# Kernel optimization log

Measured on AMD Instinct MI355X. Metric: run time of the kernel, lower is better.

Reference implementation:

```python
import jax, jax.numpy as jnp
import numpy as np

B, S, IN, OUT, H, L, NH, STEPS = 256, 128, 64, 64, 1024, 2, 4, 16
HD = H // NH


def setup_inputs() -> dict:
    key = jax.random.key(0)
    ks = iter(jax.random.split(key, 32))
    std_h = 1.0 / np.sqrt(H)

    def u(k, shape, std):
        return jax.random.uniform(k, shape, jnp.float32, -std, std)

    inp = {"x": jax.random.normal(next(ks), (B, S, IN), jnp.float32)}
    # LSTM cells: stacked gate weights, gate order (i, f, g, o); y = x@Wx + h@Wh + b
    for name, din in (("e0", IN), ("e1", H), ("d0", OUT), ("d1", H)):
        inp[name + "_Wx"] = u(next(ks), (din, 4 * H), std_h)
        inp[name + "_Wh"] = u(next(ks), (H, 4 * H), std_h)
        inp[name + "_b"] = u(next(ks), (4 * H,), std_h)
    # attention linears (x@W + b convention)
    for name in ("Wq", "Wk", "Wv", "Wo"):
        inp[name] = u(next(ks), (H, H), std_h)
    for name in ("bq", "bk", "bv", "bo"):
        inp[name] = u(next(ks), (H,), std_h)
    inp["fc_W"] = u(next(ks), (2 * H, H), 1.0 / np.sqrt(2 * H))
    inp["fc_b"] = u(next(ks), (H,), 1.0 / np.sqrt(2 * H))
    inp["out_W"] = u(next(ks), (H, OUT), std_h)
    inp["out_b"] = u(next(ks), (OUT,), std_h)
    return inp


def _cell(x_t, h, c, Wx, Wh, b):
    z = x_t @ Wx + h @ Wh + b  # [B, 4H]
    i, f, g, o = jnp.split(z, 4, axis=-1)
    c = jax.nn.sigmoid(f) * c + jax.nn.sigmoid(i) * jnp.tanh(g)
    h = jax.nn.sigmoid(o) * jnp.tanh(c)
    return h, c


def _lstm_seq(x, Wx, Wh, b):
    # x: [B, T, D] -> outputs [B, T, H], final (h, c)
    h0 = jnp.zeros((x.shape[0], H), x.dtype)
    def step(carry, xt):
        h, c = carry
        h, c = _cell(xt, h, c, Wx, Wh, b)
        return (h, c), h
    (h, c), ys = jax.lax.scan(step, (h0, h0), jnp.swapaxes(x, 0, 1))
    return jnp.swapaxes(ys, 0, 1), h, c


def reference(x, e0_Wx, e0_Wh, e0_b, e1_Wx, e1_Wh, e1_b,
              d0_Wx, d0_Wh, d0_b, d1_Wx, d1_Wh, d1_b,
              Wq, bq, Wk, bk, Wv, bv, Wo, bo, fc_W, fc_b, out_W, out_b):
    # encoder: 2-layer manual LSTM (dropout=0, eval)
    y0, h0, c0 = _lstm_seq(x, e0_Wx, e0_Wh, e0_b)
    enc_out, h1, c1 = _lstm_seq(y0, e1_Wx, e1_Wh, e1_b)

    # K/V projections of encoder outputs (constant across decoder steps)
    Kp = (enc_out @ Wk + bk).reshape(B, S, NH, HD)
    Vp = (enc_out @ Wv + bv).reshape(B, S, NH, HD)
    scale = float(HD) ** 0.5

    def dstep(carry, _):
        dh0, dc0, dh1, dc1, xin = carry
        dh0, dc0 = _cell(xin, dh0, dc0, d0_Wx, d0_Wh, d0_b)
        dh1, dc1 = _cell(dh0, dh1, dc1, d1_Wx, d1_Wh, d1_b)
        q = (dh1 @ Wq + bq).reshape(B, NH, HD)
        scores = jnp.einsum('bnd,bsnd->bns', q, Kp) / scale
        w = jax.nn.softmax(scores, axis=-1)
        ctx = jnp.einsum('bns,bsnd->bnd', w, Vp).reshape(B, H)
        attn = ctx @ Wo + bo
        comb = jax.nn.relu(jnp.concatenate([dh1, attn], axis=-1) @ fc_W + fc_b)
        out = comb @ out_W + out_b  # [B, OUT]
        return (dh0, dc0, dh1, dc1, out), out

    init = (h0, c0, h1, c1, jnp.zeros((B, OUT), x.dtype))
    _, preds = jax.lax.scan(dstep, init, None, length=STEPS)
    return jnp.swapaxes(preds, 0, 1)  # [B, STEPS, OUT]
```

## Files before the change

kernel.cpp:

```cpp
#include <hip/hip_runtime.h>
#include <math.h>

typedef _Float16 h8 __attribute__((ext_vector_type(8)));
typedef _Float16 h4 __attribute__((ext_vector_type(4)));
typedef float f16v __attribute__((ext_vector_type(16)));

#define HPS 262144
#define XPS 2097152
#define IPS 16384
#define BSTR 40
#define BUFE (128 * BSTR)

__device__ __forceinline__ float4 ld4(const float* p) { return *(const float4*)p; }
__device__ __forceinline__ float sigf(float x) { return 1.0f / (1.0f + expf(-x)); }
__device__ __forceinline__ float bf2f(unsigned short u) { return __uint_as_float(((unsigned)u) << 16); }
__device__ __forceinline__ float rdin(const void* p, size_t i, int bf) {
  return bf ? bf2f(((const unsigned short*)p)[i]) : ((const float*)p)[i];
}

__global__ void detect_dtype(const unsigned short* __restrict__ probe, int n, int* flag) {
  __shared__ int cnt;
  if (threadIdx.x == 0) cnt = 0;
  __syncthreads();
  int c = 0;
  for (int i = threadIdx.x; i < n; i += 256) {
    int e = (probe[i] >> 7) & 0xFF;
    if (e >= 100 && e <= 126) c++;
  }
  atomicAdd(&cnt, c);
  __syncthreads();
  if (threadIdx.x == 0) *flag = (cnt > (n * 3) / 4) ? 1 : 0;
}

__global__ void cvt_f32(const void* __restrict__ in, float* __restrict__ out, int n,
                        const int* __restrict__ flag) {
  int bf = *flag;
  int i = blockIdx.x * 256 + threadIdx.x;
  if (i < n) out[i] = rdin(in, i, bf);
}

__global__ void tsplit(const void* __restrict__ in, int N,
                       _Float16* __restrict__ outHi, _Float16* __restrict__ outLo,
                       int ldo, int kOff, int pOff, const int* __restrict__ flag) {
  __shared__ float tile[32][33];
  int bf = *flag;
  int kb = blockIdx.x * 32, nb = blockIdx.y * 32;
  for (int r = threadIdx.y; r < 32; r += 8)
    tile[threadIdx.x][r] = rdin(in, (size_t)(kb + r) * N + nb + threadIdx.x, bf);
  __syncthreads();
  for (int r = threadIdx.y; r < 32; r += 8) {
    float v = tile[r][threadIdx.x];
    _Float16 hi = (_Float16)v;
    _Float16 lo = (_Float16)(v - (float)hi);
    size_t o = (size_t)(pOff + nb + r) * ldo + kOff + kb + threadIdx.x;
    outHi[o] = hi; outLo[o] = lo;
  }
}

__global__ void f2h_kernel(const void* __restrict__ in, _Float16* __restrict__ out, int n,
                           const int* __restrict__ flag) {
  int bf = *flag;
  int i = blockIdx.x * 1024 + threadIdx.x * 4;
  if (i < n) {
    float vv[4];
#pragma unroll
    for (int k = 0; k < 4; ++k) vv[k] = rdin(in, i + k, bf);
    h4 hv, lv;
#pragma unroll
    for (int k = 0; k < 4; ++k) { hv[k] = (_Float16)vv[k]; lv[k] = (_Float16)(vv[k] - (float)hv[k]); }
    *(h4*)(out + i) = hv;
    *(h4*)(out + n + i) = lv;
  }
}

__global__ void sentinel_kernel(float* out, float v) { out[0] = v; }

__device__ __forceinline__ void gemm_tile(
    const _Float16* __restrict__ A0, int lda0, int aps0,
    const _Float16* __restrict__ A1, int lda1, int aps1, int ksplit,
    const _Float16* __restrict__ WTh, const _Float16* __restrict__ WTl, int ldw,
    int pbase, int c0, int c1,
    float* __restrict__ zp, int zld, _Float16* Bs ) {
  const int tid = threadIdx.x;
  const int wv = tid >> 6, lane = tid & 63;
  const int l31 = lane & 31, lhi = lane >> 5;

  f16v acc00 = {}, acc01 = {}, acc10 = {}, acc11 = {};

  const int r0 = wv * 64 + l31;
  const int r1 = r0 + 32;
  const _Float16* a0b0 = A0 + (size_t)r0 * lda0;
  const _Float16* a1b0 = A1 + (size_t)r0 * lda1;
  const _Float16* a0b1 = A0 + (size_t)r1 * lda0;
  const _Float16* a1b1 = A1 + (size_t)r1 * lda1;

  const int spl = tid >> 7;
  const int sidx = tid & 127;
  const int sp = sidx >> 1;
  const int skh = (sidx & 1) << 4;
  const _Float16* srow = (spl ? WTl : WTh) + (size_t)(pbase + sp) * ldw + skh;
  const int sdoff = (spl * 64 + sp) * BSTR + skh;

  {
    const _Float16* s = srow + (c0 << 5);
    float4 v0 = *(const float4*)(s);
    float4 v1 = *(const float4*)(s + 8);
    _Float16* d = Bs + sdoff;
    *(float4*)(d) = v0;
    *(float4*)(d + 8) = v1;
  }

  int buf = 0;
  for (int c = c0; c < c1; ++c) {
    __syncthreads();
    float4 n0, n1;
    const bool more = (c + 1 < c1);
    if (more) {
      const _Float16* s = srow + ((c + 1) << 5);
      n0 = *(const float4*)(s);
      n1 = *(const float4*)(s + 8);
    }
    const _Float16* bb = Bs + buf * BUFE;
    int k0 = c << 5;
#pragma unroll
    for (int sub = 0; sub < 2; ++sub) {
      int ks = k0 + sub * 16 + lhi * 8;
      const _Float16 *pa0, *pa1; int ap;
      if (ks < ksplit) { pa0 = a0b0 + ks; pa1 = a0b1 + ks; ap = aps0; }
      else { int kk = ks - ksplit; pa0 = a1b0 + kk; pa1 = a1b1 + kk; ap = aps1; }
      h8 af0h = *(const h8*)pa0;
      h8 af0l = *(const h8*)(pa0 + ap);
      h8 af1h = *(const h8*)pa1;
      h8 af1l = *(const h8*)(pa1 + ap);
      int kl = sub * 16 + lhi * 8;
      h8 b0h = *(const h8*)(bb + (size_t)(l31) * BSTR + kl);
      h8 b0l = *(const h8*)(bb + (size_t)(64 + l31) * BSTR + kl);
      h8 b1h = *(const h8*)(bb + (size_t)(32 + l31) * BSTR + kl);
      h8 b1l = *(const h8*)(bb + (size_t)(96 + l31) * BSTR + kl);
      acc00 = __builtin_amdgcn_mfma_f32_32x32x16_f16(af0h, b0h, acc00, 0, 0, 0);
      acc00 = __builtin_amdgcn_mfma_f32_32x32x16_f16(af0h, b0l, acc00, 0, 0, 0);
      acc00 = __builtin_amdgcn_mfma_f32_32x32x16_f16(af0l, b0h, acc00, 0, 0, 0);
      acc01 = __builtin_amdgcn_mfma_f32_32x32x16_f16(af0h, b1h, acc01, 0, 0, 0);
      acc01 = __builtin_amdgcn_mfma_f32_32x32x16_f16(af0h, b1l, acc01, 0, 0, 0);
      acc01 = __builtin_amdgcn_mfma_f32_32x32x16_f16(af0l, b1h, acc01, 0, 0, 0);
      acc10 = __builtin_amdgcn_mfma_f32_32x32x16_f16(af1h, b0h, acc10, 0, 0, 0);
      acc10 = __builtin_amdgcn_mfma_f32_32x32x16_f16(af1h, b0l, acc10, 0, 0, 0);
      acc10 = __builtin_amdgcn_mfma_f32_32x32x16_f16(af1l, b0h, acc10, 0, 0, 0);
      acc11 = __builtin_amdgcn_mfma_f32_32x32x16_f16(af1h, b1h, acc11, 0, 0, 0);
      acc11 = __builtin_amdgcn_mfma_f32_32x32x16_f16(af1h, b1l, acc11, 0, 0, 0);
      acc11 = __builtin_amdgcn_mfma_f32_32x32x16_f16(af1l, b1h, acc11, 0, 0, 0);
    }
    if (more) {
      _Float16* d = Bs + (buf ^ 1) * BUFE + sdoff;
      *(float4*)(d) = n0;
      *(float4*)(d + 8) = n1;
    }
    buf ^= 1;
  }

#pragma unroll
  for (int mi = 0; mi < 2; ++mi) {
#pragma unroll
    for (int ni = 0; ni < 2; ++ni) {
      f16v av = (mi == 0) ? (ni == 0 ? acc00 : acc01) : (ni == 0 ? acc10 : acc11);
      int col = pbase + ni * 32 + l31;
#pragma unroll
      for (int r = 0; r < 16; ++r) {
        int row = wv * 64 + mi * 32 + (r & 3) + ((r >> 2) * 8) + lhi * 4;
        zp[(size_t)row * zld + col] = av[r];
      }
    }
  }
}

__global__ __launch_bounds__(256, 2) void enc_gemm(int t, int l1kq,
    const _Float16* xh, const _Float16* h0, const _Float16* h1,
    const _Float16* wt0h, const _Float16* wt0l,
    const _Float16* wt1h, const _Float16* wt1l,
    const _Float16* wtkvh, const _Float16* wtkvl,
    float* z0, float* z1, float* kvz) {
  __shared__ _Float16 Bs[2 * BUFE];
  int blk = blockIdx.x;
  int nl1 = 64 * l1kq;
  if (blk < nl1) {
    if (t < 1 || t > 128) return;
    int pg = blk & 63, kq = blk >> 6;
    int c0 = (64 * kq) / l1kq, c1 = (64 * (kq + 1)) / l1kq;
    gemm_tile(h0, 1024, HPS, h1, 1024, HPS, 1024, wt1h, wt1l, 2048,
              pg * 64, c0, c1, z1 + (size_t)kq * 1048576, 4096, Bs);
  } else if (blk < nl1 + 128) {
    if (t > 127) return;
    int w = blk - nl1, pg = w & 63, kq = w >> 6;
    gemm_tile(xh + (size_t)t * 64, 8192, XPS, h0, 1024, HPS, 64, wt0h, wt0l, 1088,
              pg * 64, kq * 17, kq * 17 + 17, z0 + (size_t)kq * 1048576, 4096, Bs);
  } else {
    if (t < 2) return;
    int w = blk - nl1 - 128, pg = w & 31, kq = w >> 5;
    gemm_tile(h1, 1024, HPS, h1, 1024, HPS, 1024, wtkvh, wtkvl, 1024,
              pg * 64, kq * 16, kq * 16 + 16, kvz + (size_t)kq * 524288, 2048, Bs);
  }
}

__global__ __launch_bounds__(256, 2) void gemm_k(
    const _Float16* A0, int lda0, int aps0,
    const _Float16* A1, int lda1, int aps1, int ksplit,
    const _Float16* WTh, const _Float16* WTl, int ldw,
    int npg, int nkq, int tot, int kqoff, float* zp, int zld) {
  __shared__ _Float16 Bs[2 * BUFE];
  int pg = blockIdx.x % npg, kq = blockIdx.x / npg + kqoff;
  int c0 = (tot * kq) / nkq, c1 = (tot * (kq + 1)) / nkq;
  gemm_tile(A0, lda0, aps0, A1, lda1, aps1, ksplit, WTh, WTl, ldw,
            pg * 64, c0, c1, zp + (size_t)kq * 256 * zld, zld, Bs);
}

__global__ __launch_bounds__(256, 2) void qfc_kernel(
    const _Float16* h1,
    const _Float16* wqh, const _Float16* wql,
    const _Float16* wfh, const _Float16* wfl,
    float* qp, float* fcp) {
  __shared__ _Float16 Bs[2 * BUFE];
  int blk = blockIdx.x;
  if (blk < 64) {
    int pg = blk & 15, kq = blk >> 4;
    gemm_tile(h1, 1024, HPS, h1, 1024, HPS, 1024, wqh, wql, 1024,
              pg * 64, kq * 8, kq * 8 + 8, qp + (size_t)kq * 262144, 1024, Bs);
  } else {
    int w = blk - 64, pg = w & 15, kq = w >> 4;
    gemm_tile(h1, 1024, HPS, h1, 1024, HPS, 1024, wfh, wfl, 2048,
              pg * 64, kq * 8, kq * 8 + 8, fcp + (size_t)kq * 262144, 1024, Bs);
  }
}

__device__ __forceinline__ void gates_body(const float* __restrict__ zp, int nparts,
    const float* __restrict__ bias, float* __restrict__ c,
    _Float16* __restrict__ h, int blk) {
  int e = blk * 1024 + threadIdx.x * 4;
  int b = e >> 10, j = e & 1023;
  size_t zrow = (size_t)b * 4096;
  float4 vi = ld4(bias + j), vf = ld4(bias + 1024 + j), vg = ld4(bias + 2048 + j), vo = ld4(bias + 3072 + j);
  for (int q = 0; q < nparts; ++q) {
    const float* zq = zp + (size_t)q * 1048576 + zrow;
    float4 t;
    t = ld4(zq + j);        vi.x += t.x; vi.y += t.y; vi.z += t.z; vi.w += t.w;
    t = ld4(zq + 1024 + j); vf.x += t.x; vf.y += t.y; vf.z += t.z; vf.w += t.w;
    t = ld4(zq + 2048 + j); vg.x += t.x; vg.y += t.y; vg.z += t.z; vg.w += t.w;
    t = ld4(zq + 3072 + j); vo.x += t.x; vo.y += t.y; vo.z += t.z; vo.w += t.w;
  }
  float* cp = c + (size_t)b * 1024 + j;
  float4 cv = ld4(cp);
  float zi[4] = {vi.x, vi.y, vi.z, vi.w}, zf[4] = {vf.x, vf.y, vf.z, vf.w};
  float zg[4] = {vg.x, vg.y, vg.z, vg.w}, zo[4] = {vo.x, vo.y, vo.z, vo.w};
  float cc[4] = {cv.x, cv.y, cv.z, cv.w};
  float hn[4];
#pragma unroll
  for (int k = 0; k < 4; ++k) {
    float ii = sigf(zi[k]), ff = sigf(zf[k]), gg = tanhf(zg[k]), oo = sigf(zo[k]);
    float cn = ff * cc[k] + ii * gg;
    cc[k] = cn;
    hn[k] = oo * tanhf(cn);
  }
  float4 co; co.x = cc[0]; co.y = cc[1]; co.z = cc[2]; co.w = cc[3];
  *(float4*)cp = co;
  h4 hv, lv;
#pragma unroll
  for (int k = 0; k < 4; ++k) { hv[k] = (_Float16)hn[k]; lv[k] = (_Float16)(hn[k] - (float)hv[k]); }
  *(h4*)(h + (size_t)b * 1024 + j) = hv;
  *(h4*)(h + HPS + (size_t)b * 1024 + j) = lv;
}

__global__ void enc_gates(int t, int l1parts, const float* z0, const float* z1, const float* kvz,
                          const float* b0, const float* b1,
                          const float* bk, const float* bv,
                          float* c0, float* c1, _Float16* h0, _Float16* h1,
                          _Float16* Kp, _Float16* Vp) {
  int blk = blockIdx.x;
  if (blk < 256) {
    if (t > 127) return;
    gates_body(z0, 2, b0, c0, h0, blk);
  } else if (blk < 512) {
    if (t < 1 || t > 128) return;
    gates_body(z1, l1parts, b1, c1, h1, blk - 256);
  } else {
    if (t < 2) return;
    int e = (blk - 512) * 1024 + threadIdx.x * 4;
    int b = e >> 11, col = e & 2047;
    const float* bb = (col < 1024) ? (bk + col) : (bv + col - 1024);
    float4 v = ld4(bb);
    for (int q = 0; q < 2; ++q) {
      float4 tt = ld4(kvz + (size_t)q * 524288 + e);
      v.x += tt.x; v.y += tt.y; v.z += tt.z; v.w += tt.w;
    }
    _Float16* dst = (col < 1024) ? Kp : Vp;
    int cc = (col < 1024) ? col : col - 1024;
    h4 hv; hv[0] = (_Float16)v.x; hv[1] = (_Float16)v.y; hv[2] = (_Float16)v.z; hv[3] = (_Float16)v.w;
    *(h4*)(dst + (size_t)(b * 128 + (t - 2)) * 1024 + cc) = hv;
  }
}

__global__ void dec_gates(const float* zp, int nparts, const float* bias,
                          float* c, _Float16* h) {
  gates_body(zp, nparts, bias, c, h, blockIdx.x);
}

__global__ void reduce_act(const float* __restrict__ zp, int nparts,
                           const float* __restrict__ bias, _Float16* __restrict__ out, int relu) {
  int e = blockIdx.x * 1024 + threadIdx.x * 4;
  int j = e & 1023;
  float4 v = ld4(bias + j);
  for (int q = 0; q < nparts; ++q) {
    float4 t = ld4(zp + (size_t)q * 262144 + e);
    v.x += t.x; v.y += t.y; v.z += t.z; v.w += t.w;
  }
  if (relu) {
    v.x = fmaxf(v.x, 0.f); v.y = fmaxf(v.y, 0.f); v.z = fmaxf(v.z, 0.f); v.w = fmaxf(v.w, 0.f);
  }
  float vv[4] = {v.x, v.y, v.z, v.w};
  h4 hv, lv;
#pragma unroll
  for (int k = 0; k < 4; ++k) { hv[k] = (_Float16)vv[k]; lv[k] = (_Float16)(vv[k] - (float)hv[k]); }
  *(h4*)(out + e) = hv;
  *(h4*)(out + HPS + e) = lv;
}

__global__ void out_reduce(const float* __restrict__ op, const float* __restrict__ outb,
                           float* __restrict__ dout, _Float16* __restrict__ xin, int s) {
  int e = blockIdx.x * 1024 + threadIdx.x * 4;
  int b = e >> 6, o = e & 63;
  float4 v = ld4(outb + o);
  for (int q = 0; q < 16; ++q) {
    float4 t = ld4(op + (size_t)q * 16384 + e);
    v.x += t.x; v.y += t.y; v.z += t.z; v.w += t.w;
  }
  *(float4*)(dout + (size_t)(b * 16 + s) * 64 + o) = v;
  float vv[4] = {v.x, v.y, v.z, v.w};
  h4 hv, lv;
#pragma unroll
  for (int k = 0; k < 4; ++k) { hv[k] = (_Float16)vv[k]; lv[k] = (_Float16)(vv[k] - (float)hv[k]); }
  *(h4*)(xin + e) = hv;
  *(h4*)(xin + IPS + e) = lv;
}

__global__ void attn_kernel(const float* __restrict__ qp, const float* __restrict__ bq,
                            const _Float16* __restrict__ Kp, const _Float16* __restrict__ Vp,
                            _Float16* __restrict__ ctx) {
  int b = blockIdx.x >> 2, n = blockIdx.x & 3;
  __shared__ float qs[256];
  __shared__ float sw[128];
  int tid = threadIdx.x;
  float qv = bq[n * 256 + tid];
  for (int q = 0; q < 4; ++q) qv += qp[(size_t)q * 262144 + (size_t)b * 1024 + n * 256 + tid];
  qs[tid] = qv;
  __syncthreads();
  int w = tid >> 6, lane = tid & 63;
  for (int s = w; s < 128; s += 4) {
    const _Float16* kr = Kp + (size_t)(b * 128 + s) * 1024 + n * 256;
    float acc = 0.f;
#pragma unroll
    for (int d = 0; d < 4; ++d) acc += qs[lane + d * 64] * (float)kr[lane + d * 64];
    for (int off = 32; off; off >>= 1) acc += __shfl_down(acc, off);
    if (lane == 0) sw[s] = acc * 0.0625f;
  }
  __syncthreads();
  if (w == 0) {
    float a = sw[lane], bb = sw[lane + 64];
    float m = fmaxf(a, bb);
    for (int off = 32; off; off >>= 1) m = fmaxf(m, __shfl_down(m, off));
    m = __shfl(m, 0);
    float e1 = expf(a - m), e2 = expf(bb - m);
    float ss = e1 + e2;
    for (int off = 32; off; off >>= 1) ss += __shfl_down(ss, off);
    ss = __shfl(ss, 0);
    float inv = 1.0f / ss;
    sw[lane] = e1 * inv; sw[lane + 64] = e2 * inv;
  }
  __syncthreads();
  float acc = 0.f;
  const _Float16* vb = Vp + (size_t)b * 131072 + n * 256 + tid;
  for (int s2 = 0; s2 < 128; ++s2) acc += sw[s2] * (float)vb[(size_t)s2 * 1024];
  size_t idx = (size_t)b * 1024 + n * 256 + tid;
  _Float16 hi = (_Float16)acc;
  ctx[idx] = hi;
  ctx[HPS + idx] = (_Float16)(acc - (float)hi);
}

extern "C" void kernel_launch(void* const* d_in, const int* in_sizes, int n_in,
                              void* d_out, int out_size, void* d_ws, size_t ws_size,
                              hipStream_t stream) {
  const void* x     = d_in[0];
  const void* e0_Wx = d_in[1];
  const void* e0_Wh = d_in[2];
  const void* e0_b  = d_in[3];
  const void* e1_Wx = d_in[4];
  const void* e1_Wh = d_in[5];
  const void* e1_b  = d_in[6];
  const void* d0_Wx = d_in[7];
  const void* d0_Wh = d_in[8];
  const void* d0_b  = d_in[9];
  const void* d1_Wx = d_in[10];
  const void* d1_Wh = d_in[11];
  const void* d1_b  = d_in[12];
  const void* Wq = d_in[13];
  const void* Wk = d_in[14];
  const void* Wv = d_in[15];
  const void* Wo = d_in[16];
  const void* bq = d_in[17];
  const void* bk = d_in[18];
  const void* bv = d_in[19];
  const void* bo = d_in[20];
  const void* fc_W  = d_in[21];
  const void* fc_b  = d_in[22];
  const void* out_W = d_in[23];
  const void* out_b = d_in[24];

  int l1parts = 4;
  char* p = (char*)d_ws;
  int* flag; float* bias_arena; char* warena; char* zero0;
  _Float16 *h0, *h1, *xin, *Kp, *Vp, *ctx, *attn_h, *comb;
  float *c0, *c1; float* zarena;
  size_t zeroBytes = 0;

  for (int attempt = 0; attempt < 2; ++attempt) {
    p = (char*)d_ws;
    auto alloc = [&](size_t bytes) { char* r = p; p += (bytes + 255) & ~(size_t)255; return r; };
    flag = (int*)alloc(256);
    bias_arena = (float*)alloc(87040);
    warena = alloc(68419584);
    zero0 = p;
    h0 = (_Float16*)alloc(1048576);
    h1 = (_Float16*)alloc(1048576);
    c0 = (float*)alloc(1048576);
    c1 = (float*)alloc(1048576);
    xin = (_Float16*)alloc(65536);
    zeroBytes = (size_t)(p - zero0);
    Kp = (_Float16*)alloc(67108864);
    Vp = (_Float16*)alloc(67108864);
    zarena = (float*)alloc((size_t)(3 + l1parts) * 4194304);
    ctx    = (_Float16*)alloc(1048576);
    attn_h = (_Float16*)alloc(1048576);
    comb   = (_Float16*)alloc(1048576);
    if ((size_t)(p - (char*)d_ws) <= ws_size) break;
    l1parts = 2;
  }
  if ((size_t)(p - (char*)d_ws) > ws_size) {
    sentinel_kernel<<<1, 1, 0, stream>>>((float*)d_out, 1.0e9f + (float)ws_size);
    return;
  }

  float* c_e0b = bias_arena +     0;
  float* c_e1b = bias_arena +  4096;
  float* c_d0b = bias_arena +  8192;
  float* c_d1b = bias_arena + 12288;
  float* c_bq  = bias_arena + 16384;
  float* c_bk  = bias_arena + 17408;
  float* c_bv  = bias_arena + 18432;
  float* c_bo  = bias_arena + 19456;
  float* c_fcb = bias_arena + 20480;
  float* c_ob  = bias_arena + 21504;

  _Float16* wt_e0h = (_Float16*)(warena);
  _Float16* wt_e0l = (_Float16*)(warena +  8912896);
  _Float16* wt_e1h = (_Float16*)(warena + 17825792);
  _Float16* wt_e1l = (_Float16*)(warena + 34603008);
  _Float16* wt_kvh = (_Float16*)(warena + 51380224);
  _Float16* wt_kvl = (_Float16*)(warena + 55574528);
  _Float16* xh     = (_Float16*)(warena + 59768832);
  _Float16* wt_d0h = (_Float16*)(warena);
  _Float16* wt_d0l = (_Float16*)(warena +  8912896);
  _Float16* wt_d1h = (_Float16*)(warena + 17825792);
  _Float16* wt_d1l = (_Float16*)(warena + 34603008);
  _Float16* wt_qh  = (_Float16*)(warena + 51380224);
  _Float16* wt_ql  = (_Float16*)(warena + 53477376);
  _Float16* wt_oh  = (_Float16*)(warena + 55574528);
  _Float16* wt_ol  = (_Float16*)(warena + 57671680);
  _Float16* wt_fch = (_Float16*)(warena + 59768832);
  _Float16* wt_fcl = (_Float16*)(warena + 63963136);
  _Float16* wt_outh= (_Float16*)(warena + 68157440);
  _Float16* wt_outl= (_Float16*)(warena + 68288512);

  float* z0e = zarena;
  float* z1e = zarena + 2097152;
  float* kvz = z1e + (size_t)l1parts * 1048576;
  float* zdec = zarena;
  float* fcp = zarena;
  float* qp  = zarena + 2097152;
  float* op  = zarena + 3145728;

  detect_dtype<<<1, 256, 0, stream>>>((const unsigned short*)e0_Wx, 16384, flag);
  cvt_f32<<<16, 256, 0, stream>>>(e0_b, c_e0b, 4096, flag);
  cvt_f32<<<16, 256, 0, stream>>>(e1_b, c_e1b, 4096, flag);
  cvt_f32<<<16, 256, 0, stream>>>(d0_b, c_d0b, 4096, flag);
  cvt_f32<<<16, 256, 0, stream>>>(d1_b, c_d1b, 4096, flag);
  cvt_f32<<<4, 256, 0, stream>>>(bq, c_bq, 1024, flag);
  cvt_f32<<<4, 256, 0, stream>>>(bk, c_bk, 1024, flag);
  cvt_f32<<<4, 256, 0, stream>>>(bv, c_bv, 1024, flag);
  cvt_f32<<<4, 256, 0, stream>>>(bo, c_bo, 1024, flag);
  cvt_f32<<<4, 256, 0, stream>>>(fc_b, c_fcb, 1024, flag);
  cvt_f32<<<1, 64, 0, stream>>>(out_b, c_ob, 64, flag);

  dim3 tb(32, 8);
  tsplit<<<dim3(2, 128), tb, 0, stream>>>(e0_Wx, 4096, wt_e0h, wt_e0l, 1088, 0, 0, flag);
  tsplit<<<dim3(32, 128), tb, 0, stream>>>(e0_Wh, 4096, wt_e0h, wt_e0l, 1088, 64, 0, flag);
  tsplit<<<dim3(32, 128), tb, 0, stream>>>(e1_Wx, 4096, wt_e1h, wt_e1l, 2048, 0, 0, flag);
  tsplit<<<dim3(32, 128), tb, 0, stream>>>(e1_Wh, 4096, wt_e1h, wt_e1l, 2048, 1024, 0, flag);
  tsplit<<<dim3(32, 32), tb, 0, stream>>>(Wk, 1024, wt_kvh, wt_kvl, 1024, 0, 0, flag);
  tsplit<<<dim3(32, 32), tb, 0, stream>>>(Wv, 1024, wt_kvh, wt_kvl, 1024, 0, 1024, flag);
  f2h_kernel<<<2048, 256, 0, stream>>>(x, xh, 2097152, flag);
  hipMemsetAsync(zero0, 0, zeroBytes, stream);

  int encBlocks = 64 * l1parts + 192;
  for (int t = 0; t <= 129; ++t) {
    enc_gemm<<<encBlocks, 256, 0, stream>>>(t, l1parts, xh, h0, h1,
                                            wt_e0h, wt_e0l, wt_e1h, wt_e1l,
                                            wt_kvh, wt_kvl, z0e, z1e, kvz);
    enc_gates<<<1024, 256, 0, stream>>>(t, l1parts, z0e, z1e, kvz, c_e0b, c_e1b, c_bk, c_bv,
                                        c0, c1, h0, h1, Kp, Vp);
  }

  tsplit<<<dim3(2, 128), tb, 0, stream>>>(d0_Wx, 4096, wt_d0h, wt_d0l, 1088, 0, 0, flag);
  tsplit<<<dim3(32, 128), tb, 0, stream>>>(d0_Wh, 4096, wt_d0h, wt_d0l, 1088, 64, 0, flag);
  tsplit<<<dim3(32, 128), tb, 0, stream>>>(d1_Wx, 4096, wt_d1h, wt_d1l, 2048, 0, 0, flag);
  tsplit<<<dim3(32, 128), tb, 0, stream>>>(d1_Wh, 4096, wt_d1h, wt_d1l, 2048, 1024, 0, flag);
  tsplit<<<dim3(32, 32), tb, 0, stream>>>(Wq, 1024, wt_qh, wt_ql, 1024, 0, 0, flag);
  tsplit<<<dim3(32, 32), tb, 0, stream>>>(Wo, 1024, wt_oh, wt_ol, 1024, 0, 0, flag);
  tsplit<<<dim3(64, 32), tb, 0, stream>>>(fc_W, 1024, wt_fch, wt_fcl, 2048, 0, 0, flag);
  tsplit<<<dim3(32, 2), tb, 0, stream>>>(out_W, 64, wt_outh, wt_outl, 1024, 0, 0, flag);

  for (int s = 0; s < 16; ++s) {
    gemm_k<<<256, 256, 0, stream>>>(xin, 64, IPS, h0, 1024, HPS, 64,
                                    wt_d0h, wt_d0l, 1088, 64, 4, 34, 0, zdec, 4096);
    dec_gates<<<256, 256, 0, stream>>>(zdec, 4, c_d0b, c0, h0);
    gemm_k<<<256, 256, 0, stream>>>(h0, 1024, HPS, h1, 1024, HPS, 1024,
                                    wt_d1h, wt_d1l, 2048, 64, 4, 64, 0, zdec, 4096);
    dec_gates<<<256, 256, 0, stream>>>(zdec, 4, c_d1b, c1, h1);
    qfc_kernel<<<128, 256, 0, stream>>>(h1, wt_qh, wt_ql, wt_fch, wt_fcl, qp, fcp);
    attn_kernel<<<1024, 256, 0, stream>>>(qp, c_bq, Kp, Vp, ctx);
    gemm_k<<<64, 256, 0, stream>>>(ctx, 1024, HPS, ctx, 1024, HPS, 1024,
                                   wt_oh, wt_ol, 1024, 16, 4, 32, 0, qp, 1024);
    reduce_act<<<256, 256, 0, stream>>>(qp, 4, c_bo, attn_h, 0);
    gemm_k<<<64, 256, 0, stream>>>(h1, 1024, HPS, attn_h, 1024, HPS, 1024,
                                   wt_fch, wt_fcl, 2048, 16, 8, 64, 4, fcp, 1024);
    reduce_act<<<256, 256, 0, stream>>>(fcp, 8, c_fcb, comb, 1);
    gemm_k<<<16, 256, 0, stream>>>(comb, 1024, HPS, comb, 1024, HPS, 1024,
                                   wt_outh, wt_outl, 1024, 1, 16, 32, 0, op, 64);
    out_reduce<<<16, 256, 0, stream>>>(op, c_ob, (float*)d_out, xin, s);
  }
}
```

Measured before the change: 9.562 ms.

## Store fp16 activation operands in MFMA-fragment-packed layout for coalesced A loads

Activation matrices (h0, h1, x, ctx, attn_h, comb, xin) are now written in a blocked layout: 32-row by 8-k fragments stored contiguously, so each lane's 16-byte A-operand load in gemm_tile reads adjacent memory instead of striding by a full row. All producers (gates, reduce_act, out_reduce, attention, the input packing kernel) and every GEMM call site are updated to the new indexing. The aim is fewer memory transactions and better coalescing on the A side of every recurrent GEMM. The attention epilogue gains an extra shared-memory pass and barrier to pack its output.

```diff
diff --git a/kernel.cpp b/kernel.cpp
--- a/kernel.cpp
+++ b/kernel.cpp
@@ -11,11 +11,15 @@
 #define BSTR 40
 #define BUFE (128 * BSTR)
 
+
 __device__ __forceinline__ float4 ld4(const float* p) { return *(const float4*)p; }
 __device__ __forceinline__ float sigf(float x) { return 1.0f / (1.0f + expf(-x)); }
 __device__ __forceinline__ float bf2f(unsigned short u) { return __uint_as_float(((unsigned)u) << 16); }
 __device__ __forceinline__ float rdin(const void* p, size_t i, int bf) {
   return bf ? bf2f(((const unsigned short*)p)[i]) : ((const float*)p)[i];
+}
+__device__ __forceinline__ size_t pidx(int row, int k, int ldaK) {
+  return ((size_t)((row >> 5) * ldaK + (k >> 3))) * 256 + ((row & 31) << 3) + (k & 7);
 }
 
 __global__ void detect_dtype(const unsigned short* __restrict__ probe, int n, int* flag) {
@@ -57,27 +61,30 @@
   }
 }
 
-__global__ void f2h_kernel(const void* __restrict__ in, _Float16* __restrict__ out, int n,
-                           const int* __restrict__ flag) {
+__global__ void f2h_pack(const void* __restrict__ in, _Float16* __restrict__ out,
+                         const int* __restrict__ flag) {
   int bf = *flag;
-  int i = blockIdx.x * 1024 + threadIdx.x * 4;
-  if (i < n) {
-    float vv[4];
-#pragma unroll
-    for (int k = 0; k < 4; ++k) vv[k] = rdin(in, i + k, bf);
-    h4 hv, lv;
-#pragma unroll
-    for (int k = 0; k < 4; ++k) { hv[k] = (_Float16)vv[k]; lv[k] = (_Float16)(vv[k] - (float)hv[k]); }
-    *(h4*)(out + i) = hv;
-    *(h4*)(out + n + i) = lv;
-  }
+  size_t idx = ((size_t)blockIdx.x * 256 + threadIdx.x) * 8;
+  int b = (int)(idx >> 13);
+  int rem = (int)(idx & 8191);
+  int t = rem >> 6;
+  int k = rem & 63;
+  float vv[8];
+#pragma unroll
+  for (int e = 0; e < 8; ++e) vv[e] = rdin(in, idx + e, bf);
+  h8 hv, lv;
+#pragma unroll
+  for (int e = 0; e < 8; ++e) { hv[e] = (_Float16)vv[e]; lv[e] = (_Float16)(vv[e] - (float)hv[e]); }
+  size_t o = (size_t)t * 16384 + pidx(b, k, 8);
+  *(h8*)(out + o) = hv;
+  *(h8*)(out + XPS + o) = lv;
 }
 
 __global__ void sentinel_kernel(float* out, float v) { out[0] = v; }
 
 __device__ __forceinline__ void gemm_tile(
-    const _Float16* __restrict__ A0, int lda0, int aps0,
-    const _Float16* __restrict__ A1, int lda1, int aps1, int ksplit,
+    const _Float16* __restrict__ A0, int ldaK0, int aps0,
+    const _Float16* __restrict__ A1, int ldaK1, int aps1, int ksplit,
     const _Float16* __restrict__ WTh, const _Float16* __restrict__ WTl, int ldw,
     int pbase, int c0, int c1,
     float* __restrict__ zp, int zld, _Float16* Bs ) {
@@ -87,12 +94,13 @@
 
   f16v acc00 = {}, acc01 = {}, acc10 = {}, acc11 = {};
 
-  const int r0 = wv * 64 + l31;
-  const int r1 = r0 + 32;
-  const _Float16* a0b0 = A0 + (size_t)r0 * lda0;
-  const _Float16* a1b0 = A1 + (size_t)r0 * lda1;
-  const _Float16* a0b1 = A0 + (size_t)r1 * lda0;
-  const _Float16* a1b1 = A1 + (size_t)r1 * lda1;
+  const int rb0 = wv * 2;
+  const int loff = (l31 << 3) + (lhi << 8);
+  const _Float16* pA0a = A0 + ((size_t)rb0 * ldaK0) * 256 + loff;
+  const _Float16* pA0b = A0 + ((size_t)(rb0 + 1) * ldaK0) * 256 + loff;
+  const _Float16* pA1a = A1 + ((size_t)rb0 * ldaK1) * 256 + loff;
+  const _Float16* pA1b = A1 + ((size_t)(rb0 + 1) * ldaK1) * 256 + loff;
+  const int ks8 = ksplit >> 3;
 
   const int spl = tid >> 7;
   const int sidx = tid & 127;
@@ -121,17 +129,18 @@
       n1 = *(const float4*)(s + 8);
     }
     const _Float16* bb = Bs + buf * BUFE;
-    int k0 = c << 5;
+    const bool sideA = ((c << 5) < ksplit);
+    const _Float16* qa = sideA ? pA0a : pA1a;
+    const _Float16* qb = sideA ? pA0b : pA1b;
+    const int ap = sideA ? aps0 : aps1;
+    const int kb = sideA ? (c << 2) : ((c << 2) - ks8);
 #pragma unroll
     for (int sub = 0; sub < 2; ++sub) {
-      int ks = k0 + sub * 16 + lhi * 8;
-      const _Float16 *pa0, *pa1; int ap;
-      if (ks < ksplit) { pa0 = a0b0 + ks; pa1 = a0b1 + ks; ap = aps0; }
-      else { int kk = ks - ksplit; pa0 = a1b0 + kk; pa1 = a1b1 + kk; ap = aps1; }
-      h8 af0h = *(const h8*)pa0;
-      h8 af0l = *(const h8*)(pa0 + ap);
-      h8 af1h = *(const h8*)pa1;
-      h8 af1l = *(const h8*)(pa1 + ap);
+      const int off = (kb + sub * 2) << 8;
+      h8 af0h = *(const h8*)(qa + off);
+      h8 af0l = *(const h8*)(qa + off + ap);
+      h8 af1h = *(const h8*)(qb + off);
+      h8 af1l = *(const h8*)(qb + off + ap);
       int kl = sub * 16 + lhi * 8;
       h8 b0h = *(const h8*)(bb + (size_t)(l31) * BSTR + kl);
       h8 b0l = *(const h8*)(bb + (size_t)(64 + l31) * BSTR + kl);
@@ -186,30 +195,30 @@
     if (t < 1 || t > 128) return;
     int pg = blk & 63, kq = blk >> 6;
     int c0 = (64 * kq) / l1kq, c1 = (64 * (kq + 1)) / l1kq;
-    gemm_tile(h0, 1024, HPS, h1, 1024, HPS, 1024, wt1h, wt1l, 2048,
+    gemm_tile(h0, 128, HPS, h1, 128, HPS, 1024, wt1h, wt1l, 2048,
               pg * 64, c0, c1, z1 + (size_t)kq * 1048576, 4096, Bs);
   } else if (blk < nl1 + 128) {
     if (t > 127) return;
     int w = blk - nl1, pg = w & 63, kq = w >> 6;
-    gemm_tile(xh + (size_t)t * 64, 8192, XPS, h0, 1024, HPS, 64, wt0h, wt0l, 1088,
+    gemm_tile(xh + (size_t)t * 16384, 8, XPS, h0, 128, HPS, 64, wt0h, wt0l, 1088,
               pg * 64, kq * 17, kq * 17 + 17, z0 + (size_t)kq * 1048576, 4096, Bs);
   } else {
     if (t < 2) return;
     int w = blk - nl1 - 128, pg = w & 31, kq = w >> 5;
-    gemm_tile(h1, 1024, HPS, h1, 1024, HPS, 1024, wtkvh, wtkvl, 1024,
+    gemm_tile(h1, 128, HPS, h1, 128, HPS, 1024, wtkvh, wtkvl, 1024,
               pg * 64, kq * 16, kq * 16 + 16, kvz + (size_t)kq * 524288, 2048, Bs);
   }
 }
 
 __global__ __launch_bounds__(256, 2) void gemm_k(
-    const _Float16* A0, int lda0, int aps0,
-    const _Float16* A1, int lda1, int aps1, int ksplit,
+    const _Float16* A0, int ldaK0, int aps0,
+    const _Float16* A1, int ldaK1, int aps1, int ksplit,
     const _Float16* WTh, const _Float16* WTl, int ldw,
     int npg, int nkq, int tot, int kqoff, float* zp, int zld) {
   __shared__ _Float16 Bs[2 * BUFE];
   int pg = blockIdx.x % npg, kq = blockIdx.x / npg + kqoff;
   int c0 = (tot * kq) / nkq, c1 = (tot * (kq + 1)) / nkq;
-  gemm_tile(A0, lda0, aps0, A1, lda1, aps1, ksplit, WTh, WTl, ldw,
+  gemm_tile(A0, ldaK0, aps0, A1, ldaK1, aps1, ksplit, WTh, WTl, ldw,
             pg * 64, c0, c1, zp + (size_t)kq * 256 * zld, zld, Bs);
 }
 
@@ -222,11 +231,11 @@
   int blk = blockIdx.x;
   if (blk < 64) {
     int pg = blk & 15, kq = blk >> 4;
-    gemm_tile(h1, 1024, HPS, h1, 1024, HPS, 1024, wqh, wql, 1024,
+    gemm_tile(h1, 128, HPS, h1, 128, HPS, 1024, wqh, wql, 1024,
               pg * 64, kq * 8, kq * 8 + 8, qp + (size_t)kq * 262144, 1024, Bs);
   } else {
     int w = blk - 64, pg = w & 15, kq = w >> 4;
-    gemm_tile(h1, 1024, HPS, h1, 1024, HPS, 1024, wfh, wfl, 2048,
+    gemm_tile(h1, 128, HPS, h1, 128, HPS, 1024, wfh, wfl, 2048,
               pg * 64, kq * 8, kq * 8 + 8, fcp + (size_t)kq * 262144, 1024, Bs);
   }
 }
@@ -264,8 +273,9 @@
   h4 hv, lv;
 #pragma unroll
   for (int k = 0; k < 4; ++k) { hv[k] = (_Float16)hn[k]; lv[k] = (_Float16)(hn[k] - (float)hv[k]); }
-  *(h4*)(h + (size_t)b * 1024 + j) = hv;
-  *(h4*)(h + HPS + (size_t)b * 1024 + j) = lv;
+  size_t o = pidx(b, j, 128);
+  *(h4*)(h + o) = hv;
+  *(h4*)(h + HPS + o) = lv;
 }
 
 __global__ void enc_gates(int t, int l1parts, const float* z0, const float* z1, const float* kvz,
@@ -305,7 +315,7 @@
 __global__ void reduce_act(const float* __restrict__ zp, int nparts,
                            const float* __restrict__ bias, _Float16* __restrict__ out, int relu) {
   int e = blockIdx.x * 1024 + threadIdx.x * 4;
-  int j = e & 1023;
+  int b = e >> 10, j = e & 1023;
   float4 v = ld4(bias + j);
   for (int q = 0; q < nparts; ++q) {
     float4 t = ld4(zp + (size_t)q * 262144 + e);
@@ -318,8 +328,9 @@
   h4 hv, lv;
 #pragma unroll
   for (int k = 0; k < 4; ++k) { hv[k] = (_Float16)vv[k]; lv[k] = (_Float16)(vv[k] - (float)hv[k]); }
-  *(h4*)(out + e) = hv;
-  *(h4*)(out + HPS + e) = lv;
+  size_t o = pidx(b, j, 128);
+  *(h4*)(out + o) = hv;
+  *(h4*)(out + HPS + o) = lv;
 }
 
 __global__ void out_reduce(const float* __restrict__ op, const float* __restrict__ outb,
@@ -336,8 +347,9 @@
   h4 hv, lv;
 #pragma unroll
   for (int k = 0; k < 4; ++k) { hv[k] = (_Float16)vv[k]; lv[k] = (_Float16)(vv[k] - (float)hv[k]); }
-  *(h4*)(xin + e) = hv;
-  *(h4*)(xin + IPS + e) = lv;
+  size_t po = pidx(b, o, 8);
+  *(h4*)(xin + po) = hv;
+  *(h4*)(xin + IPS + po) = lv;
 }
 
 __global__ void attn_kernel(const float* __restrict__ qp, const float* __restrict__ bq,
@@ -377,10 +389,21 @@
   float acc = 0.f;
   const _Float16* vb = Vp + (size_t)b * 131072 + n * 256 + tid;
   for (int s2 = 0; s2 < 128; ++s2) acc += sw[s2] * (float)vb[(size_t)s2 * 1024];
-  size_t idx = (size_t)b * 1024 + n * 256 + tid;
-  _Float16 hi = (_Float16)acc;
-  ctx[idx] = hi;
-  ctx[HPS + idx] = (_Float16)(acc - (float)hi);
+  qs[tid] = acc;
+  __syncthreads();
+  if (tid < 32) {
+    int k0 = n * 256 + tid * 8;
+    h8 hh, hl;
+#pragma unroll
+    for (int e = 0; e < 8; ++e) {
+      float v = qs[tid * 8 + e];
+      _Float16 hi = (_Float16)v;
+      hh[e] = hi; hl[e] = (_Float16)(v - (float)hi);
+    }
+    size_t o = pidx(b, k0, 128);
+    *(h8*)(ctx + o) = hh;
+    *(h8*)(ctx + HPS + o) = hl;
+  }
 }
 
 extern "C" void kernel_launch(void* const* d_in, const int* in_sizes, int n_in,
@@ -504,7 +527,7 @@
   tsplit<<<dim3(32, 128), tb, 0, stream>>>(e1_Wh, 4096, wt_e1h, wt_e1l, 2048, 1024, 0, flag);
   tsplit<<<dim3(32, 32), tb, 0, stream>>>(Wk, 1024, wt_kvh, wt_kvl, 1024, 0, 0, flag);
   tsplit<<<dim3(32, 32), tb, 0, stream>>>(Wv, 1024, wt_kvh, wt_kvl, 1024, 0, 1024, flag);
-  f2h_kernel<<<2048, 256, 0, stream>>>(x, xh, 2097152, flag);
+  f2h_pack<<<1024, 256, 0, stream>>>(x, xh, flag);
   hipMemsetAsync(zero0, 0, zeroBytes, stream);
 
   int encBlocks = 64 * l1parts + 192;
@@ -526,21 +549,21 @@
   tsplit<<<dim3(32, 2), tb, 0, stream>>>(out_W, 64, wt_outh, wt_outl, 1024, 0, 0, flag);
 
   for (int s = 0; s < 16; ++s) {
-    gemm_k<<<256, 256, 0, stream>>>(xin, 64, IPS, h0, 1024, HPS, 64,
+    gemm_k<<<256, 256, 0, stream>>>(xin, 8, IPS, h0, 128, HPS, 64,
                                     wt_d0h, wt_d0l, 1088, 64, 4, 34, 0, zdec, 4096);
     dec_gates<<<256, 256, 0, stream>>>(zdec, 4, c_d0b, c0, h0);
-    gemm_k<<<256, 256, 0, stream>>>(h0, 1024, HPS, h1, 1024, HPS, 1024,
+    gemm_k<<<256, 256, 0, stream>>>(h0, 128, HPS, h1, 128, HPS, 1024,
                                     wt_d1h, wt_d1l, 2048, 64, 4, 64, 0, zdec, 4096);
     dec_gates<<<256, 256, 0, stream>>>(zdec, 4, c_d1b, c1, h1);
     qfc_kernel<<<128, 256, 0, stream>>>(h1, wt_qh, wt_ql, wt_fch, wt_fcl, qp, fcp);
     attn_kernel<<<1024, 256, 0, stream>>>(qp, c_bq, Kp, Vp, ctx);
-    gemm_k<<<64, 256, 0, stream>>>(ctx, 1024, HPS, ctx, 1024, HPS, 1024,
+    gemm_k<<<64, 256, 0, stream>>>(ctx, 128, HPS, ctx, 128, HPS, 1024,
                                    wt_oh, wt_ol, 1024, 16, 4, 32, 0, qp, 1024);
     reduce_act<<<256, 256, 0, stream>>>(qp, 4, c_bo, attn_h, 0);
-    gemm_k<<<64, 256, 0, stream>>>(h1, 1024, HPS, attn_h, 1024, HPS, 1024,
+    gemm_k<<<64, 256, 0, stream>>>(h1, 128, HPS, attn_h, 128, HPS, 1024,
                                    wt_fch, wt_fcl, 2048, 16, 8, 64, 4, fcp, 1024);
     reduce_act<<<256, 256, 0, stream>>>(fcp, 8, c_fcb, comb, 1);
-    gemm_k<<<16, 256, 0, stream>>>(comb, 1024, HPS, comb, 1024, HPS, 1024,
+    gemm_k<<<16, 256, 0, stream>>>(comb, 128, HPS, comb, 128, HPS, 1024,
                                    wt_outh, wt_outl, 1024, 1, 16, 32, 0, op, 64);
     out_reduce<<<16, 256, 0, stream>>>(op, c_ob, (float*)d_out, xin, s);
   }
```

After: 9.908 ms. 3.6% more time.
